# Optimization experiments

Measured on AMD Instinct MI355X. Metric: run time of the kernel, lower is better.

## Reference

```python
import jax, jax.numpy as jnp
import numpy as np

KH, KW, PAD = 3, 3, 1
K = KH * KW


def _offset_conv(x, w, b):
    # standard 3x3 conv, stride 1, padding 1, NCHW
    out = jax.lax.conv_general_dilated(
        x, w, window_strides=(1, 1), padding=((PAD, PAD), (PAD, PAD)),
        dimension_numbers=("NCHW", "OIHW", "NCHW"))
    return out + b[None, :, None, None]


def _deform_conv(x, offsets, weight, groups):
    # torchvision.ops.deform_conv2d semantics: offset channels are
    # (dy, dx) pairs per kernel tap; zero padding outside the image;
    # bilinear interpolation with per-corner validity masks.
    B, C, H, W = x.shape
    off = offsets.reshape(B, K, 2, H, W)
    dy, dx = off[:, :, 0], off[:, :, 1]                      # [B,K,H,W]

    ky, kx = jnp.meshgrid(jnp.arange(KH), jnp.arange(KW), indexing="ij")
    ky = ky.reshape(K); kx = kx.reshape(K)
    base_y = (jnp.arange(H)[None, :, None] + (ky - PAD)[:, None, None])  # [K,H,1]
    base_x = (jnp.arange(W)[None, None, :] + (kx - PAD)[:, None, None])  # [K,1,W]
    py = base_y[None].astype(x.dtype) + dy                   # [B,K,H,W]
    px = base_x[None].astype(x.dtype) + dx

    # torchvision returns 0 when the sample point is fully outside
    valid = (py > -1) & (py < H) & (px > -1) & (px < W)
    y0 = jnp.floor(py); x0 = jnp.floor(px)
    ly = py - y0; lx = px - x0                               # fractional parts
    y0i = y0.astype(jnp.int32); x0i = x0.astype(jnp.int32)

    def gather(yi, xi):
        ok = (yi >= 0) & (yi < H) & (xi >= 0) & (xi < W) & valid
        yic = jnp.clip(yi, 0, H - 1)
        xic = jnp.clip(xi, 0, W - 1)
        def per_b(img, yb, xb, okb):
            # img [C,H,W]; yb,xb,okb [K,H,W] -> [C,K,H,W]
            return img[:, yb, xb] * okb[None].astype(img.dtype)
        return jax.vmap(per_b)(x, yic, xic, ok)

    v00 = gather(y0i, x0i)
    v01 = gather(y0i, x0i + 1)
    v10 = gather(y0i + 1, x0i)
    v11 = gather(y0i + 1, x0i + 1)
    w00 = ((1 - ly) * (1 - lx))[:, None]
    w01 = ((1 - ly) * lx)[:, None]
    w10 = (ly * (1 - lx))[:, None]
    w11 = (ly * lx)[:, None]
    sampled = v00 * w00 + v01 * w01 + v10 * w10 + v11 * w11  # [B,C,K,H,W]

    Cg = C // groups
    sampled = sampled.reshape(B, groups, Cg, K, H, W)
    wg = weight.reshape(groups, Cg, Cg, K)                   # [G, Cout_g, Cin_g, K]
    out = jnp.einsum("bgckhw,gock->bgohw", sampled, wg)
    return out.reshape(B, C, H, W)


def setup_inputs() -> dict:
    key = jax.random.key(0)
    k1, k2, k3, k4 = jax.random.split(key, 4)
    B, C, H, W, groups = 4, 256, 96, 96, 4
    x = jax.random.normal(k1, (B, C, H, W), dtype=jnp.float32)
    # small offset-conv weights keep learned offsets in a realistic range
    offset_w = jax.random.normal(k2, (2 * K, C, KH, KW), dtype=jnp.float32) * 0.02
    offset_b = jax.random.normal(k3, (2 * K,), dtype=jnp.float32) * 0.1
    fan_in = (C // groups) * KH * KW
    weight = jax.random.normal(k4, (C, C // groups, KH, KW), dtype=jnp.float32) / np.sqrt(fan_in)
    return {"x": x, "offset_w": offset_w, "offset_b": offset_b,
            "weight": weight, "groups": groups}


def reference(x, offset_w, offset_b, weight, groups):
    offsets = _offset_conv(x, offset_w, offset_b)
    return _deform_conv(x, offsets, weight, groups)
```

## Files before the change

kernel.cpp:

```cpp
#include <hip/hip_runtime.h>
#include <hip/hip_bf16.h>
#include <math.h>

#define B_   4
#define C_   256
#define H_   96
#define W_   96
#define HW_  (H_ * W_)
#define G_   4
#define CG_  64
#define K_   9
#define PW_  98
#define PROW_ (PW_ * C_)

typedef __bf16  bf16x8 __attribute__((ext_vector_type(8)));
typedef float   f32x4  __attribute__((ext_vector_type(4)));

__global__ __launch_bounds__(256) void transpose_prep_kernel(
    const float* __restrict__ x, const float* __restrict__ ow,
    const float* __restrict__ wt, __hip_bfloat16* __restrict__ xtp,
    __hip_bfloat16* __restrict__ aOW, __hip_bfloat16* __restrict__ aW)
{
    int t = threadIdx.x;
    int gid = blockIdx.x * 256 + t;

    if (gid < 73728) {
        int j    = gid & 7;
        int r    = gid >> 3;
        int lane = r & 63;  r >>= 6;
        int mt   = r & 1;   r >>= 1;
        int ks   = r & 7;   r >>= 3;
        int tap  = r;
        int m = mt * 16 + (lane & 15);
        int c = ks * 32 + (lane >> 4) * 8 + j;
        float v = (m < 18) ? ow[(m * 256 + c) * 9 + tap] : 0.f;
        aOW[gid] = __float2bfloat16(v);
    }
    if (gid < 147456) {
        int j    = gid & 7;
        int r    = gid >> 3;
        int lane = r & 63;  r >>= 6;
        int ct   = r & 1;   r >>= 1;
        int half = r & 1;   r >>= 1;
        int ks   = r & 1;   r >>= 1;
        int tap  = r % 9;
        int g    = r / 9;
        int c  = ks * 32 + (lane >> 4) * 8 + j;
        int co = half * 32 + ct * 16 + (lane & 15);
        float v = wt[(((g * CG_ + co) * CG_ + c) * 9) + tap];
        aW[gid] = __float2bfloat16(v);
    }

    int blk = blockIdx.x;
    int ch  = blk & 1;
    int bh  = blk >> 1;
    int b = bh / H_, h = bh - b * H_;
    __shared__ __align__(16) __hip_bfloat16 tile[96 * 136];
    const float* xb = x + (size_t)b * C_ * HW_ + (size_t)(ch * 128) * HW_ + h * W_;
#pragma unroll
    for (int r = 0; r < 12; ++r) {
        int e4 = r * 256 + t;
        int c = e4 / 24, w4 = e4 - c * 24;
        float4 v = *(const float4*)(xb + (size_t)c * HW_ + w4 * 4);
        int base = (w4 * 4) * 136 + c;
        tile[base      ] = __float2bfloat16(v.x);
        tile[base + 136] = __float2bfloat16(v.y);
        tile[base + 272] = __float2bfloat16(v.z);
        tile[base + 408] = __float2bfloat16(v.w);
    }
    __syncthreads();
    __hip_bfloat16* ob = xtp + ((size_t)(b * PW_ + h + 1) * PW_ + 1) * C_ + ch * 128;
#pragma unroll
    for (int i = 0; i < 6; ++i) {
        int sIdx = i * 256 + t;
        int px = sIdx >> 4, seg = sIdx & 15;
        *(bf16x8*)(ob + px * 256 + seg * 8) =
            *(const bf16x8*)(&tile[px * 136 + seg * 8]);
    }
    bf16x8 z = {};
    if (t < 32) {
        int side = t >> 4, i = t & 15;
        *(bf16x8*)(xtp + ((size_t)(b * PW_ + h + 1) * PW_ + side * 97) * C_
                   + ch * 128 + i * 8) = z;
    }
    if (h == 0 || h == 95) {
        int row = (h == 0) ? 0 : 97;
        __hip_bfloat16* rb = xtp + (size_t)(b * PW_ + row) * PROW_;
        for (int i = 0; i < 7; ++i) {
            int idx = i * 256 + t;
            if (idx < 1568) *(bf16x8*)(rb + (ch * 1568 + idx) * 8) = z;
        }
    }
}

__global__ __launch_bounds__(384) void offset_conv_kernel(
    const __hip_bfloat16* __restrict__ xtp, const __hip_bfloat16* __restrict__ aOW,
    const float* __restrict__ bias, __hip_bfloat16* __restrict__ off2)
{
    int blk = blockIdx.x;
    int xcd = blk & 7;
    int s   = blk >> 3;
    int unit = xcd * 96 + s;
    int bh   = unit >> 1;
    int whalf = unit & 1;
    int b   = bh / H_, h = bh % H_;
    int t = threadIdx.x, lane = t & 63;
    int ww = __builtin_amdgcn_readfirstlane(t >> 6);
    int nt = ww % 3;
    int kh = ww / 3;
    int w0 = whalf * 48 + nt * 16;
    int ml = lane & 15, kq = lane >> 4;

    __shared__ __align__(16) f32x4 red[3 * 64 * 2];

    f32x4 acc0 = {}, acc1 = {};
    const __hip_bfloat16* xb = xtp + (size_t)b * (PW_ * PROW_);
    const __hip_bfloat16* aT = aOW + kh * 4096 + lane * 8;

    for (int tap = 0; tap < 9; ++tap) {
        int ky = tap / 3, kx = tap - ky * 3;
        const __hip_bfloat16* brow =
            xb + ((h + ky) * PW_ + (w0 + ml + kx)) * C_ + kh * 128 + kq * 8;
        const __hip_bfloat16* at = aT + tap * 8192;
#pragma unroll
        for (int ks = 0; ks < 4; ++ks) {
            bf16x8 bf = *(const bf16x8*)(brow + ks * 32);
            bf16x8 a0 = *(const bf16x8*)(at + ks * 1024);
            bf16x8 a1 = *(const bf16x8*)(at + ks * 1024 + 512);
            acc0 = __builtin_amdgcn_mfma_f32_16x16x32_bf16(a0, bf, acc0, 0, 0, 0);
            acc1 = __builtin_amdgcn_mfma_f32_16x16x32_bf16(a1, bf, acc1, 0, 0, 0);
        }
    }

    if (kh == 1) {
        red[(nt * 64 + lane) * 2 + 0] = acc0;
        red[(nt * 64 + lane) * 2 + 1] = acc1;
    }
    __syncthreads();
    if (kh == 0) {
        acc0 += red[(nt * 64 + lane) * 2 + 0];
        acc1 += red[(nt * 64 + lane) * 2 + 1];
        int w = w0 + ml;
#pragma unroll
        for (int r = 0; r < 4; ++r) {
            int j0 = kq * 4 + r;
            off2[((size_t)(b * 9 + (j0 >> 1)) * HW_ + h * W_ + w) * 2 + (j0 & 1)] =
                __float2bfloat16(acc0[r] + bias[j0]);
            int j1 = 16 + kq * 4 + r;
            if (j1 < 18)
                off2[((size_t)(b * 9 + (j1 >> 1)) * HW_ + h * W_ + w) * 2 + (j1 & 1)] =
                    __float2bfloat16(acc1[r] + bias[j1]);
        }
    }
}

__global__ __launch_bounds__(384, 4) void deform_kernel(
    const __hip_bfloat16* __restrict__ xtp, const __hip_bfloat16* __restrict__ off2,
    const __hip_bfloat16* __restrict__ aW, float* __restrict__ out)
{
    int blk = blockIdx.x;
    int xcd = blk & 7;
    int s   = blk >> 3;
    int bg  = xcd * 2 + (s / H_);
    int h   = s % H_;
    int g   = bg & 3;
    int b   = bg >> 2;
    int t    = threadIdx.x;
    int lane = t & 63;
    int wave = __builtin_amdgcn_readfirstlane(t >> 6);
    int half   = wave & 1;
    int wthird = wave >> 1;

    __shared__ __align__(16) __hip_bfloat16 sS[2][96 * 72];

    const __hip_bfloat16* xb =
        xtp + ((size_t)b * (PW_ * PW_) + PW_ + 1) * C_ + g * CG_;
    const __hip_bfloat162* offp =
        (const __hip_bfloat162*)off2 + (size_t)(b * 9) * HW_ + h * W_;
    const __hip_bfloat16* aWg = aW + (g * 9) * 4096;

    int tw8 = t >> 3;
    int j8  = (t & 7) * 8;

    f32x4 acc[2][2] = {};

    auto sample = [&](int k, int p) {
        int ky = k / 3, kx = k - ky * 3;
#pragma unroll
        for (int it = 0; it < 2; ++it) {
            int w  = it * 48 + tw8;
            __hip_bfloat162 pr = offp[k * HW_ + w];
            float py = (float)(h + ky - 1) + __bfloat162float(pr.x);
            float px = (float)(w + kx - 1) + __bfloat162float(pr.y);
            bool valid = (py > -1.f) && (py < (float)H_) &&
                         (px > -1.f) && (px < (float)W_);
            float y0f = floorf(py), x0f = floorf(px);
            float ly = py - y0f, lx = px - x0f;
            int y0 = (int)y0f, x0 = (int)x0f;
            int base = valid ? (y0 * PW_ + x0) * C_ : -(PW_ + 1) * C_;
            float wy1 = valid ? ly : 0.f;
            float wy0 = valid ? (1.f - ly) : 0.f;
            float mx0 = 1.f - lx;
            float bw00 = wy0 * mx0, bw01 = wy0 * lx;
            float bw10 = wy1 * mx0, bw11 = wy1 * lx;
            const __hip_bfloat16* p0 = xb + base + j8;
            bf16x8 c00 = *(const bf16x8*)(p0);
            bf16x8 c01 = *(const bf16x8*)(p0 + C_);
            bf16x8 c10 = *(const bf16x8*)(p0 + PROW_);
            bf16x8 c11 = *(const bf16x8*)(p0 + PROW_ + C_);
            bf16x8 r;
#pragma unroll
            for (int e = 0; e < 8; ++e) {
                float v = bw00 * (float)c00[e] + bw01 * (float)c01[e]
                        + bw10 * (float)c10[e] + bw11 * (float)c11[e];
                r[e] = (__bf16)v;
            }
            *(bf16x8*)(&sS[p][w * 72 + j8]) = r;
        }
    };

    auto mmtap = [&](int k, int p) {
        bf16x8 afrag[2][2];
        const __hip_bfloat16* at = aWg + k * 4096 + half * 1024 + lane * 8;
#pragma unroll
        for (int ks = 0; ks < 2; ++ks)
#pragma unroll
            for (int ct = 0; ct < 2; ++ct)
                afrag[ks][ct] = *(const bf16x8*)(at + ks * 2048 + ct * 512);
#pragma unroll
        for (int ks = 0; ks < 2; ++ks) {
#pragma unroll
            for (int wt = 0; wt < 2; ++wt) {
                int wrow = wthird * 32 + wt * 16 + (lane & 15);
                bf16x8 bfrag = *(const bf16x8*)(
                    &sS[p][wrow * 72 + ks * 32 + (lane >> 4) * 8]);
                acc[0][wt] = __builtin_amdgcn_mfma_f32_16x16x32_bf16(
                                 afrag[ks][0], bfrag, acc[0][wt], 0, 0, 0);
                acc[1][wt] = __builtin_amdgcn_mfma_f32_16x16x32_bf16(
                                 afrag[ks][1], bfrag, acc[1][wt], 0, 0, 0);
            }
        }
    };

    sample(0, 0);
    __syncthreads();
    for (int k = 0; k < K_; ++k) {
        if (k < K_ - 1) sample(k + 1, (k + 1) & 1);
        mmtap(k, k & 1);
        if (k < K_ - 1) __syncthreads();
    }

    float* ob = out + ((b * C_ + g * CG_ + half * 32) * HW_) + h * W_ + wthird * 32;
    int rbase = (lane >> 4) * 4;
    int ncol  = lane & 15;
#pragma unroll
    for (int ct = 0; ct < 2; ++ct)
#pragma unroll
        for (int wt = 0; wt < 2; ++wt)
#pragma unroll
            for (int r = 0; r < 4; ++r)
                __builtin_nontemporal_store(
                    acc[ct][wt][r],
                    ob + (ct * 16 + rbase + r) * HW_ + wt * 16 + ncol);
}

extern "C" void kernel_launch(void* const* d_in, const int* in_sizes, int n_in,
                              void* d_out, int out_size, void* d_ws, size_t ws_size,
                              hipStream_t stream) {
    const float* x    = (const float*)d_in[0];
    const float* ow   = (const float*)d_in[1];
    const float* obi  = (const float*)d_in[2];
    const float* wt   = (const float*)d_in[3];

    __hip_bfloat16* xtp  = (__hip_bfloat16*)d_ws;
    __hip_bfloat16* off2 = xtp + (size_t)B_ * PW_ * PW_ * C_;
    __hip_bfloat16* aW   = off2 + (size_t)B_ * 9 * HW_ * 2;
    __hip_bfloat16* aOW  = aW + 147456;

    transpose_prep_kernel<<<B_ * H_ * 2, 256, 0, stream>>>(x, ow, wt, xtp, aOW, aW);
    offset_conv_kernel<<<B_ * H_ * 2, 384, 0, stream>>>(xtp, aOW, obi, off2);
    deform_kernel<<<B_ * G_ * H_, 384, 0, stream>>>(xtp, off2, aW, (float*)d_out);
}
```

Before: 170.7 us.

## Fuse offset convolution into deform kernel, keeping offsets in shared memory

Drops the separate offset_conv kernel. Each deform block now computes the 18 offset channels for its own image row with MFMA and writes them to a shared-memory array instead of a global bf16 buffer. This removes one kernel launch and the global write and read of the offset tensor. In exchange, every row's offset convolution is recomputed once per group (four times), which adds MFMA work and L2 reads of the padded input. It also adds a block-wide barrier before sampling starts.

```diff
diff --git a/kernel.cpp b/kernel.cpp
--- a/kernel.cpp
+++ b/kernel.cpp
@@ -93,70 +93,10 @@
     }
 }
 
-__global__ __launch_bounds__(384) void offset_conv_kernel(
+__global__ __launch_bounds__(384, 4) void deform_kernel(
     const __hip_bfloat16* __restrict__ xtp, const __hip_bfloat16* __restrict__ aOW,
-    const float* __restrict__ bias, __hip_bfloat16* __restrict__ off2)
-{
-    int blk = blockIdx.x;
-    int xcd = blk & 7;
-    int s   = blk >> 3;
-    int unit = xcd * 96 + s;
-    int bh   = unit >> 1;
-    int whalf = unit & 1;
-    int b   = bh / H_, h = bh % H_;
-    int t = threadIdx.x, lane = t & 63;
-    int ww = __builtin_amdgcn_readfirstlane(t >> 6);
-    int nt = ww % 3;
-    int kh = ww / 3;
-    int w0 = whalf * 48 + nt * 16;
-    int ml = lane & 15, kq = lane >> 4;
-
-    __shared__ __align__(16) f32x4 red[3 * 64 * 2];
-
-    f32x4 acc0 = {}, acc1 = {};
-    const __hip_bfloat16* xb = xtp + (size_t)b * (PW_ * PROW_);
-    const __hip_bfloat16* aT = aOW + kh * 4096 + lane * 8;
-
-    for (int tap = 0; tap < 9; ++tap) {
-        int ky = tap / 3, kx = tap - ky * 3;
-        const __hip_bfloat16* brow =
-            xb + ((h + ky) * PW_ + (w0 + ml + kx)) * C_ + kh * 128 + kq * 8;
-        const __hip_bfloat16* at = aT + tap * 8192;
-#pragma unroll
-        for (int ks = 0; ks < 4; ++ks) {
-            bf16x8 bf = *(const bf16x8*)(brow + ks * 32);
-            bf16x8 a0 = *(const bf16x8*)(at + ks * 1024);
-            bf16x8 a1 = *(const bf16x8*)(at + ks * 1024 + 512);
-            acc0 = __builtin_amdgcn_mfma_f32_16x16x32_bf16(a0, bf, acc0, 0, 0, 0);
-            acc1 = __builtin_amdgcn_mfma_f32_16x16x32_bf16(a1, bf, acc1, 0, 0, 0);
-        }
-    }
-
-    if (kh == 1) {
-        red[(nt * 64 + lane) * 2 + 0] = acc0;
-        red[(nt * 64 + lane) * 2 + 1] = acc1;
-    }
-    __syncthreads();
-    if (kh == 0) {
-        acc0 += red[(nt * 64 + lane) * 2 + 0];
-        acc1 += red[(nt * 64 + lane) * 2 + 1];
-        int w = w0 + ml;
-#pragma unroll
-        for (int r = 0; r < 4; ++r) {
-            int j0 = kq * 4 + r;
-            off2[((size_t)(b * 9 + (j0 >> 1)) * HW_ + h * W_ + w) * 2 + (j0 & 1)] =
-                __float2bfloat16(acc0[r] + bias[j0]);
-            int j1 = 16 + kq * 4 + r;
-            if (j1 < 18)
-                off2[((size_t)(b * 9 + (j1 >> 1)) * HW_ + h * W_ + w) * 2 + (j1 & 1)] =
-                    __float2bfloat16(acc1[r] + bias[j1]);
-        }
-    }
-}
-
-__global__ __launch_bounds__(384, 4) void deform_kernel(
-    const __hip_bfloat16* __restrict__ xtp, const __hip_bfloat16* __restrict__ off2,
-    const __hip_bfloat16* __restrict__ aW, float* __restrict__ out)
+    const float* __restrict__ bias, const __hip_bfloat16* __restrict__ aW,
+    float* __restrict__ out)
 {
     int blk = blockIdx.x;
     int xcd = blk & 7;
@@ -172,11 +112,56 @@
     int wthird = wave >> 1;
 
     __shared__ __align__(16) __hip_bfloat16 sS[2][96 * 72];
-
-    const __hip_bfloat16* xb =
-        xtp + ((size_t)b * (PW_ * PW_) + PW_ + 1) * C_ + g * CG_;
-    const __hip_bfloat162* offp =
-        (const __hip_bfloat162*)off2 + (size_t)(b * 9) * HW_ + h * W_;
+    __shared__ __align__(8)  __hip_bfloat162 offL[9][96];
+
+    const __hip_bfloat16* xb0 = xtp + (size_t)b * (PW_ * PROW_);
+
+    {
+        int nt = wave;
+        int ml = lane & 15, kq = lane >> 4;
+        f32x4 a0A = {}, a0B = {}, a1A = {}, a1B = {};
+        for (int tap = 0; tap < 9; ++tap) {
+            int ky = tap / 3, kx = tap - ky * 3;
+            const __hip_bfloat16* brow =
+                xb0 + ((h + ky) * PW_ + (nt * 16 + ml + kx)) * C_ + kq * 8;
+            const __hip_bfloat16* at = aOW + tap * 8192 + lane * 8;
+#pragma unroll
+            for (int ks = 0; ks < 4; ++ks) {
+                bf16x8 bf = *(const bf16x8*)(brow + ks * 32);
+                bf16x8 a0 = *(const bf16x8*)(at + ks * 1024);
+                bf16x8 a1 = *(const bf16x8*)(at + ks * 1024 + 512);
+                a0A = __builtin_amdgcn_mfma_f32_16x16x32_bf16(a0, bf, a0A, 0, 0, 0);
+                a1A = __builtin_amdgcn_mfma_f32_16x16x32_bf16(a1, bf, a1A, 0, 0, 0);
+            }
+#pragma unroll
+            for (int ks = 4; ks < 8; ++ks) {
+                bf16x8 bf = *(const bf16x8*)(brow + ks * 32);
+                bf16x8 a0 = *(const bf16x8*)(at + ks * 1024);
+                bf16x8 a1 = *(const bf16x8*)(at + ks * 1024 + 512);
+                a0B = __builtin_amdgcn_mfma_f32_16x16x32_bf16(a0, bf, a0B, 0, 0, 0);
+                a1B = __builtin_amdgcn_mfma_f32_16x16x32_bf16(a1, bf, a1B, 0, 0, 0);
+            }
+        }
+        f32x4 acc0 = a0A; acc0 += a0B;
+        f32x4 acc1 = a1A; acc1 += a1B;
+        int w = nt * 16 + ml;
+        __hip_bfloat162 p0, p1;
+        p0.x = __float2bfloat16(acc0[0] + bias[kq * 4 + 0]);
+        p0.y = __float2bfloat16(acc0[1] + bias[kq * 4 + 1]);
+        p1.x = __float2bfloat16(acc0[2] + bias[kq * 4 + 2]);
+        p1.y = __float2bfloat16(acc0[3] + bias[kq * 4 + 3]);
+        offL[kq * 2 + 0][w] = p0;
+        offL[kq * 2 + 1][w] = p1;
+        if (kq == 0) {
+            __hip_bfloat162 p8;
+            p8.x = __float2bfloat16(acc1[0] + bias[16]);
+            p8.y = __float2bfloat16(acc1[1] + bias[17]);
+            offL[8][w] = p8;
+        }
+    }
+    __syncthreads();
+
+    const __hip_bfloat16* xb = xb0 + (PW_ + 1) * C_ + g * CG_;
     const __hip_bfloat16* aWg = aW + (g * 9) * 4096;
 
     int tw8 = t >> 3;
@@ -189,7 +174,7 @@
 #pragma unroll
         for (int it = 0; it < 2; ++it) {
             int w  = it * 48 + tw8;
-            __hip_bfloat162 pr = offp[k * HW_ + w];
+            __hip_bfloat162 pr = offL[k][w];
             float py = (float)(h + ky - 1) + __bfloat162float(pr.x);
             float px = (float)(w + kx - 1) + __bfloat162float(pr.y);
             bool valid = (py > -1.f) && (py < (float)H_) &&
@@ -272,12 +257,10 @@
     const float* obi  = (const float*)d_in[2];
     const float* wt   = (const float*)d_in[3];
 
-    __hip_bfloat16* xtp  = (__hip_bfloat16*)d_ws;
-    __hip_bfloat16* off2 = xtp + (size_t)B_ * PW_ * PW_ * C_;
-    __hip_bfloat16* aW   = off2 + (size_t)B_ * 9 * HW_ * 2;
-    __hip_bfloat16* aOW  = aW + 147456;
+    __hip_bfloat16* xtp = (__hip_bfloat16*)d_ws;
+    __hip_bfloat16* aW  = xtp + (size_t)B_ * PW_ * PW_ * C_;
+    __hip_bfloat16* aOW = aW + 147456;
 
     transpose_prep_kernel<<<B_ * H_ * 2, 256, 0, stream>>>(x, ow, wt, xtp, aOW, aW);
-    offset_conv_kernel<<<B_ * H_ * 2, 384, 0, stream>>>(xtp, aOW, obi, off2);
-    deform_kernel<<<B_ * G_ * H_, 384, 0, stream>>>(xtp, off2, aW, (float*)d_out);
+    deform_kernel<<<B_ * G_ * H_, 384, 0, stream>>>(xtp, aOW, obi, aW, (float*)d_out);
 }
```

Result: slower. 261.8 us (+53.4%).
